# Optimization experiments

Measured on AMD Instinct MI355X. Metric: run time of the kernel, lower is better.

The kernel has to match this reference:

```python
import jax, jax.numpy as jnp
import numpy as np

MASK_VALUE = -1000000.0  # matches torch sequence_mask fill value


def setup_inputs() -> dict:
    key = jax.random.key(0)
    k1, k2, k3, k4 = jax.random.split(key, 4)
    B, Tq, Tk, d = 16, 2048, 2048, 128
    queries = jax.random.normal(k1, (B, Tq, d), dtype=jnp.float32)
    keys = jax.random.normal(k2, (B, Tk, d), dtype=jnp.float32)
    values = jax.random.normal(k3, (B, Tk, d), dtype=jnp.float32)
    valid_lens = jax.random.randint(k4, (B, Tq), 0, Tk, dtype=jnp.int64)
    return {"queries": queries, "keys": keys, "values": values,
            "valid_lens": valid_lens}


def reference(queries, keys, values, valid_lens):
    d = queries.shape[-1]
    Tk = keys.shape[1]
    # scores: [B, Tq, Tk]
    scores = jnp.einsum('bqd,bkd->bqk', queries, keys) / jnp.sqrt(
        jnp.asarray(d, dtype=queries.dtype))
    # per-row length mask: position k is valid iff k < valid_lens[b, q]
    mask = jnp.arange(Tk)[None, None, :] < valid_lens[:, :, None]
    scores = jnp.where(mask, scores, jnp.asarray(MASK_VALUE, scores.dtype))
    attn = jax.nn.softmax(scores, axis=-1)
    # dropout p=0.0 -> identity
    return jnp.einsum('bqk,bkd->bqd', attn, values)
```

## Files before the change

### kernel.cpp

```cpp
#include <hip/hip_runtime.h>
#include <stdint.h>
#include <math.h>

#define NB 16
#define TQ 2048
#define TK 2048
#define DH 128
#define KT (TK / 64)
#define QB (TQ / 64)

#define QK_STR 136
#define VT_STR 72
#define P_STR  72

typedef __attribute__((ext_vector_type(8))) short bf16x8;
typedef __attribute__((ext_vector_type(4))) float f32x4;
typedef __attribute__((ext_vector_type(8))) unsigned short u16x8;

__device__ __forceinline__ unsigned short f2b(float f) {
  union { float f; uint32_t u; } v; v.f = f;
  uint32_t u = v.u;
  return (unsigned short)((u + 0x7fffu + ((u >> 16) & 1u)) >> 16);
}

__device__ __forceinline__ u16x8 cvt8(const float* p) {
  const f32x4 a = *(const f32x4*)p;
  const f32x4 b = *(const f32x4*)(p + 4);
  u16x8 o;
#pragma unroll
  for (int j = 0; j < 4; ++j) { o[j] = f2b(a[j]); o[4 + j] = f2b(b[j]); }
  return o;
}

__device__ __forceinline__ int eff_len(const int* vlen, bool is64, int idx) {
  int v = is64 ? vlen[2 * idx] : vlen[idx];
  v = (v < 0) ? 0 : ((v > TK) ? TK : v);
  return (v == 0) ? TK : v;
}

__global__ __launch_bounds__(256) void sort_kernel(const int* __restrict__ vlen,
                                                   int* __restrict__ perm) {
  __shared__ int cnt_[TK + 1];
  __shared__ int base_[TK + 1];
  __shared__ int psum[256];
  const int b = blockIdx.x;
  const int t = threadIdx.x;

  int hw = 0;
#pragma unroll
  for (int i = 0; i < 8; ++i) hw |= vlen[2 * i + 1];
  const bool is64 = (hw == 0);

  for (int i = t; i <= TK; i += 256) cnt_[i] = 0;
  __syncthreads();

  int eff[8];
#pragma unroll
  for (int j = 0; j < 8; ++j) {
    const int q = j * 256 + t;
    eff[j] = eff_len(vlen, is64, b * TQ + q);
    atomicAdd(&cnt_[eff[j]], 1);
  }
  __syncthreads();

  int loc[8]; int s = 0;
#pragma unroll
  for (int j = 0; j < 8; ++j) { loc[j] = cnt_[TK - (t * 8 + j)]; s += loc[j]; }
  psum[t] = s;
  __syncthreads();
  if (t == 0) {
    int acc = 0;
    for (int i = 0; i < 256; ++i) { const int x = psum[i]; psum[i] = acc; acc += x; }
  }
  __syncthreads();
  int run = psum[t];
#pragma unroll
  for (int j = 0; j < 8; ++j) { base_[TK - (t * 8 + j)] = run; run += loc[j]; }
  __syncthreads();
#pragma unroll
  for (int j = 0; j < 8; ++j) {
    const int rank = atomicAdd(&base_[eff[j]], 1);
    perm[b * TQ + rank] = j * 256 + t;
  }
}

__global__ __launch_bounds__(256) void prep_kernel(const float* __restrict__ K,
                                                   const float* __restrict__ V,
                                                   unsigned short* __restrict__ Kb,
                                                   unsigned short* __restrict__ Vt) {
  __shared__ alignas(16) unsigned short tile[64][136];
  const int t = threadIdx.x;
  const int b = blockIdx.y;
  const int kt = blockIdx.x;
  const int k0 = kt * 64;

  const float* Ks = K + ((size_t)b * TK + k0) * DH;
  unsigned short* Kd = Kb + ((size_t)b * TK + k0) * DH;
#pragma unroll
  for (int i = 0; i < 4; ++i) {
    const int row = i * 16 + (t >> 4);
    const int c0 = (t & 15) * 8;
    *(u16x8*)(Kd + (size_t)row * DH + c0) = cvt8(Ks + (size_t)row * DH + c0);
  }
  const float* Vs = V + ((size_t)b * TK + k0) * DH;
#pragma unroll
  for (int i = 0; i < 4; ++i) {
    const int row = i * 16 + (t >> 4);
    const int c0 = (t & 15) * 8;
    *(u16x8*)(&tile[row][c0]) = cvt8(Vs + (size_t)row * DH + c0);
  }
  __syncthreads();
  {
    const int d = t >> 1;
    const int half = t & 1;
    alignas(16) unsigned short tmp[32];
#pragma unroll
    for (int j = 0; j < 32; ++j) tmp[j] = tile[half * 32 + j][d];
    unsigned short* dst = Vt + ((size_t)(b * KT + kt) * DH + d) * 64 + half * 32;
#pragma unroll
    for (int j = 0; j < 4; ++j)
      *(u16x8*)(dst + j * 8) = *(const u16x8*)(&tmp[j * 8]);
  }
}

__global__ __launch_bounds__(256) void attn_ws(const float* __restrict__ Q,
                                               const unsigned short* __restrict__ Kp,
                                               const unsigned short* __restrict__ Vp,
                                               const int* __restrict__ vlen,
                                               const int* __restrict__ perm,
                                               float* __restrict__ pO,
                                               float* __restrict__ pL,
                                               float* __restrict__ out,
                                               const int nchs) {
  __shared__ alignas(16) char smem[53248];
  __shared__ int s_bvl[4];
  unsigned short* sQ = (unsigned short*)smem;
  unsigned short* sK = (unsigned short*)(smem + 17408);
  unsigned short* sV = (unsigned short*)(smem + 34816);

  const int tid  = threadIdx.x;
  const int w    = tid >> 6;
  const int lane = tid & 63;
  const int quad = lane >> 4;
  const int l15  = lane & 15;
  const int b    = blockIdx.y;
  const int nch  = 1 << nchs;
  const int ctl  = 5 - nchs;
  const int ctiles = KT >> nchs;
  const int jq     = blockIdx.x >> nchs;
  const int cchunk = blockIdx.x & (nch - 1);
  const int q0 = jq * 64;
  const int qw = q0 + w * 16;

  int hw = 0;
#pragma unroll
  for (int i = 0; i < 8; ++i) hw |= vlen[2 * i + 1];
  const bool is64 = (hw == 0);

  const float kScaleL2 = 0.08838834764831845f * 1.4426950408889634f;
  const float kBias    = -32.0f;
  const float kKill    = -1.0e7f;

  int bvl, wvl;
  if (perm) {
    bvl = eff_len(vlen, is64, b * TQ + perm[b * TQ + q0]);
    wvl = eff_len(vlen, is64, b * TQ + perm[b * TQ + qw]);
  } else {
    int m = 0;
#pragma unroll
    for (int r = 0; r < 4; ++r)
      m = max(m, eff_len(vlen, is64, b * TQ + qw + quad * 4 + r));
    m = max(m, __shfl_xor(m, 16, 64));
    m = max(m, __shfl_xor(m, 32, 64));
    if (lane == 0) s_bvl[w] = m;
    __syncthreads();
    bvl = max(max(s_bvl[0], s_bvl[1]), max(s_bvl[2], s_bvl[3]));
    wvl = m;
  }

  const int nt = (bvl + 63) >> 6;
  const int t0 = cchunk * ctiles;
  const int t1 = (nt < t0 + ctiles) ? nt : (t0 + ctiles);
  if (t0 >= t1) return;
  const int nact = (nt + ctiles - 1) >> ctl;

  int vlr[4]; float scl[4]; int qidx[4];
#pragma unroll
  for (int r = 0; r < 4; ++r) {
    const int rank = qw + quad * 4 + r;
    const int qrow = perm ? perm[b * TQ + rank] : rank;
    qidx[r] = qrow;
    const int idx = b * TQ + qrow;
    int v = is64 ? vlen[2 * idx] : vlen[idx];
    v = (v < 0) ? 0 : ((v > TK) ? TK : v);
    scl[r] = (v == 0) ? 0.0f : kScaleL2;
    vlr[r] = (v == 0) ? TK : v;
  }

#pragma unroll
  for (int i = 0; i < 4; ++i) {
    const int row = i * 16 + (tid >> 4);
    const int qi = perm ? perm[b * TQ + q0 + row] : (q0 + row);
    const int c0 = (tid & 15) * 8;
    *(u16x8*)(sQ + row * QK_STR + c0) = cvt8(Q + ((size_t)b * TQ + qi) * DH + c0);
  }
  __syncthreads();

  bf16x8 qa[4];
  {
    const unsigned short* qrow = sQ + (w * 16 + l15) * QK_STR;
#pragma unroll
    for (int kc = 0; kc < 4; ++kc)
      qa[kc] = *(const bf16x8*)(qrow + (kc * 4 + quad) * 8);
  }
  unsigned short* sP = (unsigned short*)smem + w * (16 * P_STR);

  f32x4 Of[8] = {};
  float l_r[4] = {0.f, 0.f, 0.f, 0.f};

  const unsigned short* Kbase = Kp + (size_t)b * TK * DH;
  const unsigned short* Vbase = Vp + (size_t)(b * KT) * DH * 64;
  const int krow = tid >> 4;
  const int kch  = tid & 15;

  u16x8 kreg[4], vreg[4];
  {
    const unsigned short* Ksrc = Kbase + (size_t)t0 * 64 * DH;
#pragma unroll
    for (int i = 0; i < 4; ++i)
      kreg[i] = *(const u16x8*)(Ksrc + (size_t)(i * 16 + krow) * DH + kch * 8);
    const unsigned short* Vsrc = Vbase + (size_t)t0 * (DH * 64);
#pragma unroll
    for (int i = 0; i < 4; ++i)
      vreg[i] = *(const u16x8*)(Vsrc + (i * 256 + tid) * 8);
  }

  for (int t = t0; t < t1; ++t) {
#pragma unroll
    for (int i = 0; i < 4; ++i)
      *(u16x8*)(sK + (i * 16 + krow) * QK_STR + kch * 8) = kreg[i];
#pragma unroll
    for (int i = 0; i < 4; ++i) {
      const int chunk = i * 256 + tid;
      *(u16x8*)(sV + (chunk >> 3) * VT_STR + (chunk & 7) * 8) = vreg[i];
    }
    __syncthreads();

    if (t + 1 < t1) {
      const unsigned short* Ksrc = Kbase + (size_t)(t + 1) * 64 * DH;
#pragma unroll
      for (int i = 0; i < 4; ++i)
        kreg[i] = *(const u16x8*)(Ksrc + (size_t)(i * 16 + krow) * DH + kch * 8);
      const unsigned short* Vsrc = Vbase + (size_t)(t + 1) * (DH * 64);
#pragma unroll
      for (int i = 0; i < 4; ++i)
        vreg[i] = *(const u16x8*)(Vsrc + (i * 256 + tid) * 8);
    }

    const int k0 = t * 64;
    if (k0 < wvl) {
      f32x4 sc[4] = {};
#pragma unroll
      for (int ct = 0; ct < 4; ++ct) {
        const unsigned short* kr = sK + (ct * 16 + l15) * QK_STR;
#pragma unroll
        for (int kc = 0; kc < 4; ++kc) {
          const bf16x8 kf = *(const bf16x8*)(kr + (kc * 4 + quad) * 8);
          sc[ct] = __builtin_amdgcn_mfma_f32_16x16x32_bf16(qa[kc], kf, sc[ct], 0, 0, 0);
        }
      }

      unsigned short pb[4][4];
#pragma unroll
      for (int ct = 0; ct < 4; ++ct) {
        const int kpos = k0 + ct * 16 + l15;
#pragma unroll
        for (int r = 0; r < 4; ++r) {
          const float s = (kpos < vlr[r]) ? fmaf(sc[ct][r], scl[r], kBias) : kKill;
          const float p = exp2f(s);
          l_r[r] += p;
          pb[ct][r] = f2b(p);
        }
      }

#pragma unroll
      for (int ct = 0; ct < 4; ++ct)
#pragma unroll
        for (int r = 0; r < 4; ++r)
          sP[(quad * 4 + r) * P_STR + ct * 16 + l15] = pb[ct][r];
      __asm__ __volatile__("" ::: "memory");

      bf16x8 pa[2];
      {
        const unsigned short* pr = sP + l15 * P_STR;
#pragma unroll
        for (int ch = 0; ch < 2; ++ch)
          pa[ch] = *(const bf16x8*)(pr + (ch * 4 + quad) * 8);
      }

#pragma unroll
      for (int dt = 0; dt < 8; ++dt) {
        const unsigned short* vr = sV + (dt * 16 + l15) * VT_STR;
#pragma unroll
        for (int ch = 0; ch < 2; ++ch) {
          const bf16x8 vf = *(const bf16x8*)(vr + (ch * 4 + quad) * 8);
          Of[dt] = __builtin_amdgcn_mfma_f32_16x16x32_bf16(pa[ch], vf, Of[dt], 0, 0, 0);
        }
      }
    }
    __syncthreads();
  }

#pragma unroll
  for (int off = 1; off <= 8; off <<= 1)
#pragma unroll
    for (int r = 0; r < 4; ++r)
      l_r[r] += __shfl_xor(l_r[r], off, 64);

  if (nact == 1) {
#pragma unroll
    for (int r = 0; r < 4; ++r) {
      const float inv = 1.0f / l_r[r];
      float* orow = out + ((size_t)b * TQ + qidx[r]) * DH;
#pragma unroll
      for (int dt = 0; dt < 8; ++dt)
        orow[dt * 16 + l15] = Of[dt][r] * inv;
    }
    return;
  }

  const int slot = (b * QB + jq) * nch + cchunk;
  float* po = pO + (size_t)slot * (64 * DH);
  float* pl = pL + (size_t)slot * 64;
#pragma unroll
  for (int r = 0; r < 4; ++r) {
    const int row = w * 16 + quad * 4 + r;
#pragma unroll
    for (int dt = 0; dt < 8; ++dt)
      po[(size_t)row * DH + dt * 16 + l15] = Of[dt][r];
  }
  if (l15 == 0) {
#pragma unroll
    for (int r = 0; r < 4; ++r)
      pl[w * 16 + quad * 4 + r] = l_r[r];
  }
}

__global__ __launch_bounds__(256) void combine_kernel(const float* __restrict__ pO,
                                                      const float* __restrict__ pL,
                                                      const int* __restrict__ perm,
                                                      const int* __restrict__ vlen,
                                                      float* __restrict__ out,
                                                      const int nchs) {
  const int b = blockIdx.y;
  const int j = blockIdx.x;
  const int t = threadIdx.x;
  const int nch = 1 << nchs;
  const int ctl = 5 - nchs;

  int hw = 0;
#pragma unroll
  for (int i = 0; i < 8; ++i) hw |= vlen[2 * i + 1];
  const bool is64 = (hw == 0);

  const int bvl = eff_len(vlen, is64, b * TQ + perm[b * TQ + j * 64]);
  const int nt = (bvl + 63) >> 6;
  const int nact = (nt + (1 << ctl) - 1) >> ctl;
  if (nact <= 1) return;

  const int qboff = (b * QB + j) * nch;
#pragma unroll
  for (int i = 0; i < 8; ++i) {
    const int u = i * 256 + t;
    const int r = u >> 5;
    const int d4 = (u & 31) * 4;
    float lsum = 0.0f;
    f32x4 acc = {0.f, 0.f, 0.f, 0.f};
    for (int c = 0; c < nact; ++c) {
      lsum += pL[(size_t)(qboff + c) * 64 + r];
      acc += *(const f32x4*)(pO + ((size_t)(qboff + c) * 64 + r) * DH + d4);
    }
    const float inv = 1.0f / lsum;
    const int qi = perm[b * TQ + j * 64 + r];
    *(f32x4*)(out + ((size_t)b * TQ + qi) * DH + d4) = acc * inv;
  }
}

__global__ __launch_bounds__(256) void attn_fb(const float* __restrict__ Q,
                                               const float* __restrict__ Kp,
                                               const float* __restrict__ Vp,
                                               const int* __restrict__ vlen,
                                               float* __restrict__ out) {
  __shared__ alignas(16) char smem[53248];
  __shared__ int s_bvl[4];
  unsigned short* sQ = (unsigned short*)smem;
  unsigned short* sK = (unsigned short*)(smem + 17408);
  unsigned short* sV = (unsigned short*)(smem + 34816);

  const int tid  = threadIdx.x;
  const int w    = tid >> 6;
  const int lane = tid & 63;
  const int quad = lane >> 4;
  const int l15  = lane & 15;
  const int b    = blockIdx.y;
  const int q0   = blockIdx.x * 64;

  const float* Qb = Q + ((size_t)b * TQ + q0) * DH;
#pragma unroll
  for (int i = 0; i < 4; ++i) {
    const int row = i * 16 + (tid >> 4);
    const int c0 = (tid & 15) * 8;
    *(u16x8*)(sQ + row * QK_STR + c0) = cvt8(Qb + (size_t)row * DH + c0);
  }

  int hw = 0;
#pragma unroll
  for (int i = 0; i < 8; ++i) hw |= vlen[2 * i + 1];
  const bool is64 = (hw == 0);

  const float kScaleL2 = 0.08838834764831845f * 1.4426950408889634f;
  const float kBias    = -32.0f;
  const float kKill    = -1.0e7f;

  const int qw = q0 + w * 16;
  int vlr[4];
  float scl[4];
#pragma unroll
  for (int r = 0; r < 4; ++r) {
    const int idx = b * TQ + qw + quad * 4 + r;
    int v = is64 ? vlen[2 * idx] : vlen[idx];
    v = (v < 0) ? 0 : ((v > TK) ? TK : v);
    scl[r] = (v == 0) ? 0.0f : kScaleL2;
    vlr[r] = (v == 0) ? TK : v;
  }
  int wvl = 0;
#pragma unroll
  for (int r = 0; r < 4; ++r) wvl = max(wvl, vlr[r]);
  wvl = max(wvl, __shfl_xor(wvl, 16, 64));
  wvl = max(wvl, __shfl_xor(wvl, 32, 64));
  if (lane == 0) s_bvl[w] = wvl;
  __syncthreads();
  const int bvl = max(max(s_bvl[0], s_bvl[1]), max(s_bvl[2], s_bvl[3]));
  const int nt = (bvl + 63) >> 6;

  bf16x8 qa[4];
  {
    const unsigned short* qrow = sQ + (w * 16 + l15) * QK_STR;
#pragma unroll
    for (int kc = 0; kc < 4; ++kc)
      qa[kc] = *(const bf16x8*)(qrow + (kc * 4 + quad) * 8);
  }
  unsigned short* sP = (unsigned short*)smem + w * (16 * P_STR);

  f32x4 Of[8] = {};
  float l_r[4] = {0.f, 0.f, 0.f, 0.f};

  const float* Kb = Kp + (size_t)b * TK * DH;
  const float* Vb = Vp + (size_t)b * TK * DH;

  for (int t = 0; t < nt; ++t) {
    const int k0 = t * 64;
    __syncthreads();
#pragma unroll
    for (int i = 0; i < 4; ++i) {
      const int row = i * 16 + (tid >> 4);
      const int c0 = (tid & 15) * 8;
      *(u16x8*)(sK + row * QK_STR + c0) = cvt8(Kb + (size_t)(k0 + row) * DH + c0);
    }
#pragma unroll
    for (int i = 0; i < 4; ++i) {
      const int row = i * 16 + (tid >> 4);
      const int c0 = (tid & 15) * 8;
      *(u16x8*)(sV + row * QK_STR + c0) = cvt8(Vb + (size_t)(k0 + row) * DH + c0);
    }
    __syncthreads();
    if (k0 >= wvl) continue;

    f32x4 sc[4] = {};
#pragma unroll
    for (int ct = 0; ct < 4; ++ct) {
      const unsigned short* kr = sK + (ct * 16 + l15) * QK_STR;
#pragma unroll
      for (int kc = 0; kc < 4; ++kc) {
        const bf16x8 kf = *(const bf16x8*)(kr + (kc * 4 + quad) * 8);
        sc[ct] = __builtin_amdgcn_mfma_f32_16x16x32_bf16(qa[kc], kf, sc[ct], 0, 0, 0);
      }
    }
    unsigned short pb[4][4];
#pragma unroll
    for (int ct = 0; ct < 4; ++ct) {
      const int kpos = k0 + ct * 16 + l15;
#pragma unroll
      for (int r = 0; r < 4; ++r) {
        const float s = (kpos < vlr[r]) ? fmaf(sc[ct][r], scl[r], kBias) : kKill;
        const float p = exp2f(s);
        l_r[r] += p;
        pb[ct][r] = f2b(p);
      }
    }
#pragma unroll
    for (int ct = 0; ct < 4; ++ct)
#pragma unroll
      for (int r = 0; r < 4; ++r)
        sP[(quad * 4 + r) * P_STR + ct * 16 + l15] = pb[ct][r];
    __asm__ __volatile__("" ::: "memory");
    bf16x8 pa[2];
    {
      const unsigned short* pr = sP + l15 * P_STR;
#pragma unroll
      for (int ch = 0; ch < 2; ++ch)
        pa[ch] = *(const bf16x8*)(pr + (ch * 4 + quad) * 8);
    }
#pragma unroll
    for (int dt = 0; dt < 8; ++dt) {
      const int col = dt * 16 + l15;
#pragma unroll
      for (int ch = 0; ch < 2; ++ch) {
        bf16x8 vf;
#pragma unroll
        for (int j = 0; j < 8; ++j) {
          const int k = ch * 32 + quad * 8 + j;
          vf[j] = ((const short*)sV)[k * QK_STR + col];
        }
        Of[dt] = __builtin_amdgcn_mfma_f32_16x16x32_bf16(pa[ch], vf, Of[dt], 0, 0, 0);
      }
    }
  }

#pragma unroll
  for (int off = 1; off <= 8; off <<= 1)
#pragma unroll
    for (int r = 0; r < 4; ++r)
      l_r[r] += __shfl_xor(l_r[r], off, 64);

#pragma unroll
  for (int r = 0; r < 4; ++r) {
    const float inv = 1.0f / l_r[r];
    const int q = qw + quad * 4 + r;
    float* orow = out + ((size_t)b * TQ + q) * DH;
#pragma unroll
    for (int dt = 0; dt < 8; ++dt)
      orow[dt * 16 + l15] = Of[dt][r] * inv;
  }
}

extern "C" void kernel_launch(void* const* d_in, const int* in_sizes, int n_in,
                              void* d_out, int out_size, void* d_ws, size_t ws_size,
                              hipStream_t stream) {
  const float* Q = (const float*)d_in[0];
  const float* K = (const float*)d_in[1];
  const float* V = (const float*)d_in[2];
  const int* vl  = (const int*)d_in[3];
  float* out     = (float*)d_out;

  const size_t kb    = (size_t)NB * TK * DH;
  const size_t kvB   = kb * 2 * 2;
  const size_t permB = (size_t)NB * TQ * sizeof(int);
  const size_t baseB = kvB + permB;

  int nchs = -1;
  size_t pLB = 0;
  for (int s = 2; s >= 0; --s) {
    const size_t nch = (size_t)1 << s;
    const size_t plb = (size_t)NB * QB * nch * 64 * sizeof(float);
    const size_t pob = (size_t)NB * QB * nch * 64 * DH * sizeof(float);
    const size_t need = (s > 0) ? (baseB + plb + pob) : baseB;
    if (ws_size >= need) { nchs = s; pLB = plb; break; }
  }

  if (nchs >= 0) {
    unsigned short* Kb = (unsigned short*)d_ws;
    unsigned short* Vt = Kb + kb;
    int*   perm = (int*)((char*)d_ws + kvB);
    float* pL   = (nchs > 0) ? (float*)((char*)d_ws + baseB) : nullptr;
    float* pO   = (nchs > 0) ? (float*)((char*)d_ws + baseB + pLB) : nullptr;
    sort_kernel<<<dim3(NB), 256, 0, stream>>>(vl, perm);
    prep_kernel<<<dim3(KT, NB), 256, 0, stream>>>(K, V, Kb, Vt);
    attn_ws<<<dim3(QB << nchs, NB), 256, 0, stream>>>(Q, Kb, Vt, vl, perm,
                                                      pO, pL, out, nchs);
    if (nchs > 0)
      combine_kernel<<<dim3(QB, NB), 256, 0, stream>>>(pO, pL, perm, vl, out, nchs);
  } else if (ws_size >= kvB) {
    unsigned short* Kb = (unsigned short*)d_ws;
    unsigned short* Vt = Kb + kb;
    prep_kernel<<<dim3(KT, NB), 256, 0, stream>>>(K, V, Kb, Vt);
    attn_ws<<<dim3(QB, NB), 256, 0, stream>>>(Q, Kb, Vt, vl, nullptr,
                                              nullptr, nullptr, out, 0);
  } else {
    attn_fb<<<dim3(QB, NB), 256, 0, stream>>>(Q, K, V, vl, out);
  }
}
```

Measured before the change: 207.5 us.

## Convert split-K attention to persistent kernel with atomic job queue

Replaces the grid of one block per (query block, key chunk) with a fixed set of 512 persistent blocks. Each block pulls jobs from a global atomic counter that sort_kernel resets. Jobs are ordered chunk-major, then query block, then batch, which is meant to balance the uneven per-row work caused by sorted valid lengths and to cut launch and tail imbalance. The cost is one atomic and two barriers per job, plus the loss of the fallback that ran without a split workspace.

```diff
diff --git a/kernel.cpp b/kernel.cpp
--- a/kernel.cpp
+++ b/kernel.cpp
@@ -9,6 +9,12 @@
 #define KT (TK / 64)
 #define QB (TQ / 64)
 
+#define CT   8
+#define CTL  3
+#define NCH  4
+#define NJOBS (NB * QB * NCH)
+#define PBLK 512
+
 #define QK_STR 136
 #define VT_STR 72
 #define P_STR  72
@@ -39,12 +45,15 @@
 }
 
 __global__ __launch_bounds__(256) void sort_kernel(const int* __restrict__ vlen,
-                                                   int* __restrict__ perm) {
+                                                   int* __restrict__ perm,
+                                                   int* __restrict__ tick) {
   __shared__ int cnt_[TK + 1];
   __shared__ int base_[TK + 1];
   __shared__ int psum[256];
   const int b = blockIdx.x;
   const int t = threadIdx.x;
+
+  if (tick && b == 0 && t == 0) tick[0] = 0;
 
   int hw = 0;
 #pragma unroll
@@ -123,17 +132,17 @@
   }
 }
 
-__global__ __launch_bounds__(256) void attn_ws(const float* __restrict__ Q,
-                                               const unsigned short* __restrict__ Kp,
-                                               const unsigned short* __restrict__ Vp,
-                                               const int* __restrict__ vlen,
-                                               const int* __restrict__ perm,
-                                               float* __restrict__ pO,
-                                               float* __restrict__ pL,
-                                               float* __restrict__ out,
-                                               const int nchs) {
+__global__ __launch_bounds__(256) void attn_pers(const float* __restrict__ Q,
+                                                 const unsigned short* __restrict__ Kp,
+                                                 const unsigned short* __restrict__ Vp,
+                                                 const int* __restrict__ vlen,
+                                                 const int* __restrict__ perm,
+                                                 float* __restrict__ pO,
+                                                 float* __restrict__ pL,
+                                                 float* __restrict__ out,
+                                                 int* __restrict__ tick) {
   __shared__ alignas(16) char smem[53248];
-  __shared__ int s_bvl[4];
+  __shared__ int s_job;
   unsigned short* sQ = (unsigned short*)smem;
   unsigned short* sK = (unsigned short*)(smem + 17408);
   unsigned short* sV = (unsigned short*)(smem + 34816);
@@ -143,14 +152,8 @@
   const int lane = tid & 63;
   const int quad = lane >> 4;
   const int l15  = lane & 15;
-  const int b    = blockIdx.y;
-  const int nch  = 1 << nchs;
-  const int ctl  = 5 - nchs;
-  const int ctiles = KT >> nchs;
-  const int jq     = blockIdx.x >> nchs;
-  const int cchunk = blockIdx.x & (nch - 1);
-  const int q0 = jq * 64;
-  const int qw = q0 + w * 16;
+  const int krow = tid >> 4;
+  const int kch  = tid & 15;
 
   int hw = 0;
 #pragma unroll
@@ -161,188 +164,185 @@
   const float kBias    = -32.0f;
   const float kKill    = -1.0e7f;
 
-  int bvl, wvl;
-  if (perm) {
-    bvl = eff_len(vlen, is64, b * TQ + perm[b * TQ + q0]);
-    wvl = eff_len(vlen, is64, b * TQ + perm[b * TQ + qw]);
-  } else {
-    int m = 0;
-#pragma unroll
-    for (int r = 0; r < 4; ++r)
-      m = max(m, eff_len(vlen, is64, b * TQ + qw + quad * 4 + r));
-    m = max(m, __shfl_xor(m, 16, 64));
-    m = max(m, __shfl_xor(m, 32, 64));
-    if (lane == 0) s_bvl[w] = m;
+  for (;;) {
     __syncthreads();
-    bvl = max(max(s_bvl[0], s_bvl[1]), max(s_bvl[2], s_bvl[3]));
-    wvl = m;
-  }
-
-  const int nt = (bvl + 63) >> 6;
-  const int t0 = cchunk * ctiles;
-  const int t1 = (nt < t0 + ctiles) ? nt : (t0 + ctiles);
-  if (t0 >= t1) return;
-  const int nact = (nt + ctiles - 1) >> ctl;
-
-  int vlr[4]; float scl[4]; int qidx[4];
-#pragma unroll
-  for (int r = 0; r < 4; ++r) {
-    const int rank = qw + quad * 4 + r;
-    const int qrow = perm ? perm[b * TQ + rank] : rank;
-    qidx[r] = qrow;
-    const int idx = b * TQ + qrow;
-    int v = is64 ? vlen[2 * idx] : vlen[idx];
-    v = (v < 0) ? 0 : ((v > TK) ? TK : v);
-    scl[r] = (v == 0) ? 0.0f : kScaleL2;
-    vlr[r] = (v == 0) ? TK : v;
-  }
-
-#pragma unroll
-  for (int i = 0; i < 4; ++i) {
-    const int row = i * 16 + (tid >> 4);
-    const int qi = perm ? perm[b * TQ + q0 + row] : (q0 + row);
-    const int c0 = (tid & 15) * 8;
-    *(u16x8*)(sQ + row * QK_STR + c0) = cvt8(Q + ((size_t)b * TQ + qi) * DH + c0);
-  }
-  __syncthreads();
-
-  bf16x8 qa[4];
-  {
-    const unsigned short* qrow = sQ + (w * 16 + l15) * QK_STR;
-#pragma unroll
-    for (int kc = 0; kc < 4; ++kc)
-      qa[kc] = *(const bf16x8*)(qrow + (kc * 4 + quad) * 8);
-  }
-  unsigned short* sP = (unsigned short*)smem + w * (16 * P_STR);
-
-  f32x4 Of[8] = {};
-  float l_r[4] = {0.f, 0.f, 0.f, 0.f};
-
-  const unsigned short* Kbase = Kp + (size_t)b * TK * DH;
-  const unsigned short* Vbase = Vp + (size_t)(b * KT) * DH * 64;
-  const int krow = tid >> 4;
-  const int kch  = tid & 15;
-
-  u16x8 kreg[4], vreg[4];
-  {
-    const unsigned short* Ksrc = Kbase + (size_t)t0 * 64 * DH;
-#pragma unroll
-    for (int i = 0; i < 4; ++i)
-      kreg[i] = *(const u16x8*)(Ksrc + (size_t)(i * 16 + krow) * DH + kch * 8);
-    const unsigned short* Vsrc = Vbase + (size_t)t0 * (DH * 64);
-#pragma unroll
-    for (int i = 0; i < 4; ++i)
-      vreg[i] = *(const u16x8*)(Vsrc + (i * 256 + tid) * 8);
-  }
-
-  for (int t = t0; t < t1; ++t) {
-#pragma unroll
-    for (int i = 0; i < 4; ++i)
-      *(u16x8*)(sK + (i * 16 + krow) * QK_STR + kch * 8) = kreg[i];
+    if (tid == 0) s_job = atomicAdd(tick, 1);
+    __syncthreads();
+    const int job = s_job;
+    if (job >= NJOBS) return;
+
+    const int cchunk = job >> 9;
+    const int jq     = (job >> 4) & 31;
+    const int b      = job & 15;
+    const int q0 = jq * 64;
+    const int qw = q0 + w * 16;
+
+    const int bvl = eff_len(vlen, is64, b * TQ + perm[b * TQ + q0]);
+    const int wvl = eff_len(vlen, is64, b * TQ + perm[b * TQ + qw]);
+    const int nt = (bvl + 63) >> 6;
+    const int t0 = cchunk * CT;
+    const int t1 = (nt < t0 + CT) ? nt : (t0 + CT);
+    if (t0 >= t1) continue;
+    const int nact = (nt + CT - 1) >> CTL;
+
+    int vlr[4]; float scl[4]; int qidx[4];
+#pragma unroll
+    for (int r = 0; r < 4; ++r) {
+      const int rank = qw + quad * 4 + r;
+      const int qrow = perm[b * TQ + rank];
+      qidx[r] = qrow;
+      const int idx = b * TQ + qrow;
+      int v = is64 ? vlen[2 * idx] : vlen[idx];
+      v = (v < 0) ? 0 : ((v > TK) ? TK : v);
+      scl[r] = (v == 0) ? 0.0f : kScaleL2;
+      vlr[r] = (v == 0) ? TK : v;
+    }
+
 #pragma unroll
     for (int i = 0; i < 4; ++i) {
-      const int chunk = i * 256 + tid;
-      *(u16x8*)(sV + (chunk >> 3) * VT_STR + (chunk & 7) * 8) = vreg[i];
+      const int row = i * 16 + (tid >> 4);
+      const int qi = perm[b * TQ + q0 + row];
+      const int c0 = (tid & 15) * 8;
+      *(u16x8*)(sQ + row * QK_STR + c0) = cvt8(Q + ((size_t)b * TQ + qi) * DH + c0);
     }
     __syncthreads();
 
-    if (t + 1 < t1) {
-      const unsigned short* Ksrc = Kbase + (size_t)(t + 1) * 64 * DH;
+    bf16x8 qa[4];
+    {
+      const unsigned short* qrow = sQ + (w * 16 + l15) * QK_STR;
+#pragma unroll
+      for (int kc = 0; kc < 4; ++kc)
+        qa[kc] = *(const bf16x8*)(qrow + (kc * 4 + quad) * 8);
+    }
+    unsigned short* sP = (unsigned short*)smem + w * (16 * P_STR);
+
+    f32x4 Of[8] = {};
+    float l_r[4] = {0.f, 0.f, 0.f, 0.f};
+
+    const unsigned short* Kbase = Kp + (size_t)b * TK * DH;
+    const unsigned short* Vbase = Vp + (size_t)(b * KT) * DH * 64;
+
+    u16x8 kreg[4], vreg[4];
+    {
+      const unsigned short* Ksrc = Kbase + (size_t)t0 * 64 * DH;
 #pragma unroll
       for (int i = 0; i < 4; ++i)
         kreg[i] = *(const u16x8*)(Ksrc + (size_t)(i * 16 + krow) * DH + kch * 8);
-      const unsigned short* Vsrc = Vbase + (size_t)(t + 1) * (DH * 64);
+      const unsigned short* Vsrc = Vbase + (size_t)t0 * (DH * 64);
 #pragma unroll
       for (int i = 0; i < 4; ++i)
         vreg[i] = *(const u16x8*)(Vsrc + (i * 256 + tid) * 8);
     }
 
-    const int k0 = t * 64;
-    if (k0 < wvl) {
-      f32x4 sc[4] = {};
-#pragma unroll
-      for (int ct = 0; ct < 4; ++ct) {
-        const unsigned short* kr = sK + (ct * 16 + l15) * QK_STR;
-#pragma unroll
-        for (int kc = 0; kc < 4; ++kc) {
-          const bf16x8 kf = *(const bf16x8*)(kr + (kc * 4 + quad) * 8);
-          sc[ct] = __builtin_amdgcn_mfma_f32_16x16x32_bf16(qa[kc], kf, sc[ct], 0, 0, 0);
+    for (int t = t0; t < t1; ++t) {
+#pragma unroll
+      for (int i = 0; i < 4; ++i)
+        *(u16x8*)(sK + (i * 16 + krow) * QK_STR + kch * 8) = kreg[i];
+#pragma unroll
+      for (int i = 0; i < 4; ++i) {
+        const int chunk = i * 256 + tid;
+        *(u16x8*)(sV + (chunk >> 3) * VT_STR + (chunk & 7) * 8) = vreg[i];
+      }
+      __syncthreads();
+
+      if (t + 1 < t1) {
+        const unsigned short* Ksrc = Kbase + (size_t)(t + 1) * 64 * DH;
+#pragma unroll
+        for (int i = 0; i < 4; ++i)
+          kreg[i] = *(const u16x8*)(Ksrc + (size_t)(i * 16 + krow) * DH + kch * 8);
+        const unsigned short* Vsrc = Vbase + (size_t)(t + 1) * (DH * 64);
+#pragma unroll
+        for (int i = 0; i < 4; ++i)
+          vreg[i] = *(const u16x8*)(Vsrc + (i * 256 + tid) * 8);
+      }
+
+      const int k0 = t * 64;
+      if (k0 < wvl) {
+        f32x4 sc[4] = {};
+#pragma unroll
+        for (int ct = 0; ct < 4; ++ct) {
+          const unsigned short* kr = sK + (ct * 16 + l15) * QK_STR;
+#pragma unroll
+          for (int kc = 0; kc < 4; ++kc) {
+            const bf16x8 kf = *(const bf16x8*)(kr + (kc * 4 + quad) * 8);
+            sc[ct] = __builtin_amdgcn_mfma_f32_16x16x32_bf16(qa[kc], kf, sc[ct], 0, 0, 0);
+          }
         }
-      }
-
-      unsigned short pb[4][4];
-#pragma unroll
-      for (int ct = 0; ct < 4; ++ct) {
-        const int kpos = k0 + ct * 16 + l15;
-#pragma unroll
-        for (int r = 0; r < 4; ++r) {
-          const float s = (kpos < vlr[r]) ? fmaf(sc[ct][r], scl[r], kBias) : kKill;
-          const float p = exp2f(s);
-          l_r[r] += p;
-          pb[ct][r] = f2b(p);
+
+        unsigned short pb[4][4];
+#pragma unroll
+        for (int ct = 0; ct < 4; ++ct) {
+          const int kpos = k0 + ct * 16 + l15;
+#pragma unroll
+          for (int r = 0; r < 4; ++r) {
+            const float s = (kpos < vlr[r]) ? fmaf(sc[ct][r], scl[r], kBias) : kKill;
+            const float p = exp2f(s);
+            l_r[r] += p;
+            pb[ct][r] = f2b(p);
+          }
         }
-      }
-
-#pragma unroll
-      for (int ct = 0; ct < 4; ++ct)
-#pragma unroll
-        for (int r = 0; r < 4; ++r)
-          sP[(quad * 4 + r) * P_STR + ct * 16 + l15] = pb[ct][r];
-      __asm__ __volatile__("" ::: "memory");
-
-      bf16x8 pa[2];
-      {
-        const unsigned short* pr = sP + l15 * P_STR;
-#pragma unroll
-        for (int ch = 0; ch < 2; ++ch)
-          pa[ch] = *(const bf16x8*)(pr + (ch * 4 + quad) * 8);
-      }
-
-#pragma unroll
-      for (int dt = 0; dt < 8; ++dt) {
-        const unsigned short* vr = sV + (dt * 16 + l15) * VT_STR;
-#pragma unroll
-        for (int ch = 0; ch < 2; ++ch) {
-          const bf16x8 vf = *(const bf16x8*)(vr + (ch * 4 + quad) * 8);
-          Of[dt] = __builtin_amdgcn_mfma_f32_16x16x32_bf16(pa[ch], vf, Of[dt], 0, 0, 0);
+
+#pragma unroll
+        for (int ct = 0; ct < 4; ++ct)
+#pragma unroll
+          for (int r = 0; r < 4; ++r)
+            sP[(quad * 4 + r) * P_STR + ct * 16 + l15] = pb[ct][r];
+        __asm__ __volatile__("" ::: "memory");
+
+        bf16x8 pa[2];
+        {
+          const unsigned short* pr = sP + l15 * P_STR;
+#pragma unroll
+          for (int ch = 0; ch < 2; ++ch)
+            pa[ch] = *(const bf16x8*)(pr + (ch * 4 + quad) * 8);
         }
-      }
-    }
-    __syncthreads();
-  }
-
-#pragma unroll
-  for (int off = 1; off <= 8; off <<= 1)
-#pragma unroll
-    for (int r = 0; r < 4; ++r)
-      l_r[r] += __shfl_xor(l_r[r], off, 64);
-
-  if (nact == 1) {
+
+#pragma unroll
+        for (int dt = 0; dt < 8; ++dt) {
+          const unsigned short* vr = sV + (dt * 16 + l15) * VT_STR;
+#pragma unroll
+          for (int ch = 0; ch < 2; ++ch) {
+            const bf16x8 vf = *(const bf16x8*)(vr + (ch * 4 + quad) * 8);
+            Of[dt] = __builtin_amdgcn_mfma_f32_16x16x32_bf16(pa[ch], vf, Of[dt], 0, 0, 0);
+          }
+        }
+      }
+      __syncthreads();
+    }
+
+#pragma unroll
+    for (int off = 1; off <= 8; off <<= 1)
+#pragma unroll
+      for (int r = 0; r < 4; ++r)
+        l_r[r] += __shfl_xor(l_r[r], off, 64);
+
+    if (nact == 1) {
+#pragma unroll
+      for (int r = 0; r < 4; ++r) {
+        const float inv = 1.0f / l_r[r];
+        float* orow = out + ((size_t)b * TQ + qidx[r]) * DH;
+#pragma unroll
+        for (int dt = 0; dt < 8; ++dt)
+          orow[dt * 16 + l15] = Of[dt][r] * inv;
+      }
+      continue;
+    }
+
+    const int slot = (b * QB + jq) * NCH + cchunk;
+    float* po = pO + (size_t)slot * (64 * DH);
+    float* pl = pL + (size_t)slot * 64;
 #pragma unroll
     for (int r = 0; r < 4; ++r) {
-      const float inv = 1.0f / l_r[r];
-      float* orow = out + ((size_t)b * TQ + qidx[r]) * DH;
+      const int row = w * 16 + quad * 4 + r;
 #pragma unroll
       for (int dt = 0; dt < 8; ++dt)
-        orow[dt * 16 + l15] = Of[dt][r] * inv;
-    }
-    return;
-  }
-
-  const int slot = (b * QB + jq) * nch + cchunk;
-  float* po = pO + (size_t)slot * (64 * DH);
-  float* pl = pL + (size_t)slot * 64;
-#pragma unroll
-  for (int r = 0; r < 4; ++r) {
-    const int row = w * 16 + quad * 4 + r;
-#pragma unroll
-    for (int dt = 0; dt < 8; ++dt)
-      po[(size_t)row * DH + dt * 16 + l15] = Of[dt][r];
-  }
-  if (l15 == 0) {
-#pragma unroll
-    for (int r = 0; r < 4; ++r)
-      pl[w * 16 + quad * 4 + r] = l_r[r];
+        po[(size_t)row * DH + dt * 16 + l15] = Of[dt][r];
+    }
+    if (l15 == 0) {
+#pragma unroll
+      for (int r = 0; r < 4; ++r)
+        pl[w * 16 + quad * 4 + r] = l_r[r];
+    }
   }
 }
 
@@ -350,13 +350,10 @@
                                                       const float* __restrict__ pL,
                                                       const int* __restrict__ perm,
                                                       const int* __restrict__ vlen,
-                                                      float* __restrict__ out,
-                                                      const int nchs) {
+                                                      float* __restrict__ out) {
   const int b = blockIdx.y;
   const int j = blockIdx.x;
   const int t = threadIdx.x;
-  const int nch = 1 << nchs;
-  const int ctl = 5 - nchs;
 
   int hw = 0;
 #pragma unroll
@@ -365,10 +362,10 @@
 
   const int bvl = eff_len(vlen, is64, b * TQ + perm[b * TQ + j * 64]);
   const int nt = (bvl + 63) >> 6;
-  const int nact = (nt + (1 << ctl) - 1) >> ctl;
+  const int nact = (nt + CT - 1) >> CTL;
   if (nact <= 1) return;
 
-  const int qboff = (b * QB + j) * nch;
+  const int qboff = (b * QB + j) * NCH;
 #pragma unroll
   for (int i = 0; i < 8; ++i) {
     const int u = i * 256 + t;
@@ -556,36 +553,21 @@
   const size_t kb    = (size_t)NB * TK * DH;
   const size_t kvB   = kb * 2 * 2;
   const size_t permB = (size_t)NB * TQ * sizeof(int);
-  const size_t baseB = kvB + permB;
-
-  int nchs = -1;
-  size_t pLB = 0;
-  for (int s = 2; s >= 0; --s) {
-    const size_t nch = (size_t)1 << s;
-    const size_t plb = (size_t)NB * QB * nch * 64 * sizeof(float);
-    const size_t pob = (size_t)NB * QB * nch * 64 * DH * sizeof(float);
-    const size_t need = (s > 0) ? (baseB + plb + pob) : baseB;
-    if (ws_size >= need) { nchs = s; pLB = plb; break; }
-  }
-
-  if (nchs >= 0) {
+  const size_t tickB = 256;
+  const size_t pLB   = (size_t)NB * QB * NCH * 64 * sizeof(float);
+  const size_t pOB   = (size_t)NB * QB * NCH * 64 * DH * sizeof(float);
+
+  if (ws_size >= kvB + permB + tickB + pLB + pOB) {
     unsigned short* Kb = (unsigned short*)d_ws;
     unsigned short* Vt = Kb + kb;
     int*   perm = (int*)((char*)d_ws + kvB);
-    float* pL   = (nchs > 0) ? (float*)((char*)d_ws + baseB) : nullptr;
-    float* pO   = (nchs > 0) ? (float*)((char*)d_ws + baseB + pLB) : nullptr;
-    sort_kernel<<<dim3(NB), 256, 0, stream>>>(vl, perm);
+    int*   tick = (int*)((char*)d_ws + kvB + permB);
+    float* pL   = (float*)((char*)d_ws + kvB + permB + tickB);
+    float* pO   = (float*)((char*)d_ws + kvB + permB + tickB + pLB);
+    sort_kernel<<<dim3(NB), 256, 0, stream>>>(vl, perm, tick);
     prep_kernel<<<dim3(KT, NB), 256, 0, stream>>>(K, V, Kb, Vt);
-    attn_ws<<<dim3(QB << nchs, NB), 256, 0, stream>>>(Q, Kb, Vt, vl, perm,
-                                                      pO, pL, out, nchs);
-    if (nchs > 0)
-      combine_kernel<<<dim3(QB, NB), 256, 0, stream>>>(pO, pL, perm, vl, out, nchs);
-  } else if (ws_size >= kvB) {
-    unsigned short* Kb = (unsigned short*)d_ws;
-    unsigned short* Vt = Kb + kb;
-    prep_kernel<<<dim3(KT, NB), 256, 0, stream>>>(K, V, Kb, Vt);
-    attn_ws<<<dim3(QB, NB), 256, 0, stream>>>(Q, Kb, Vt, vl, nullptr,
-                                              nullptr, nullptr, out, 0);
+    attn_pers<<<dim3(PBLK), 256, 0, stream>>>(Q, Kb, Vt, vl, perm, pO, pL, out, tick);
+    combine_kernel<<<dim3(QB, NB), 256, 0, stream>>>(pO, pL, perm, vl, out);
   } else {
     attn_fb<<<dim3(QB, NB), 256, 0, stream>>>(Q, K, V, vl, out);
   }
```

New measurement: 179.3 us. 1.16x faster.
